# Optimization experiments

Hardware: AMD Instinct MI355X
Metric: run time of the kernel (lower is better)

## Reference

```python
import jax, jax.numpy as jnp
import numpy as np

C64 = jnp.complex64


def _ry(t):  # scalar angle -> [2,2] complex
    c = jnp.cos(t / 2).astype(C64)
    s = jnp.sin(t / 2).astype(C64)
    return jnp.stack([jnp.stack([c, -s]), jnp.stack([s, c])])


def _rz(t):  # scalar angle -> [2,2] complex (diagonal)
    p = jnp.exp(-0.5j * t.astype(C64))
    z = jnp.zeros((), C64)
    return jnp.stack([jnp.stack([p, z]), jnp.stack([z, jnp.conj(p)])])


def _rx_batch(t):  # t: [B] -> [B,2,2] complex (per-sample RX encoding gate)
    c = jnp.cos(t / 2).astype(C64)
    s = jnp.sin(t / 2).astype(C64)
    row0 = jnp.stack([c, -1j * s], axis=-1)
    row1 = jnp.stack([-1j * s, c], axis=-1)
    return jnp.stack([row0, row1], axis=-2)


def _apply_1q(state, gate, wire, n):
    # state: [B, 2^n]; wire 0 is the most significant bit (PennyLane convention)
    B = state.shape[0]
    pre, post = 2 ** wire, 2 ** (n - wire - 1)
    s = state.reshape(B, pre, 2, post)
    if gate.ndim == 2:
        s = jnp.einsum('ij,bpjq->bpiq', gate, s)
    else:  # per-sample gate [B,2,2]
        s = jnp.einsum('bij,bpjq->bpiq', gate, s)
    return s.reshape(B, -1)


def _apply_cnot(state, wire, n):
    # CNOT with control=wire, target=wire+1 (adjacent wires)
    B = state.shape[0]
    pre, post = 2 ** wire, 2 ** (n - wire - 2)
    s = state.reshape(B, pre, 2, 2, post)
    # control==1 block gets its target axis flipped
    s = jnp.concatenate([s[:, :, :1], s[:, :, 1:, ::-1]], axis=2)
    return s.reshape(B, -1)


def _circuit(x, params):
    # Batched statevector simulation of: RX(x_i) encoding, then n_layers of
    # (RY,RZ,RY) per wire + CNOT chain, then <Z_i> per wire.
    B, n = x.shape
    L = params.shape[0]
    state = jnp.zeros((B, 2 ** n), C64).at[:, 0].set(1.0)
    for i in range(n):
        state = _apply_1q(state, _rx_batch(x[:, i]), i, n)
    for l in range(L):
        for i in range(n):
            # RY(p0) first, then RZ(p1), then RY(p2): fuse into one 2x2 gate
            g = _ry(params[l, i, 2]) @ _rz(params[l, i, 1]) @ _ry(params[l, i, 0])
            state = _apply_1q(state, g, i, n)
        for i in range(n - 1):
            state = _apply_cnot(state, i, n)
    probs = jnp.abs(state) ** 2  # [B, 2^n] float32
    ez = []
    for i in range(n):
        p = probs.reshape(B, 2 ** i, 2, 2 ** (n - i - 1))
        ez.append(p[:, :, 0].sum((1, 2)) - p[:, :, 1].sum((1, 2)))
    return jnp.stack(ez, axis=1)  # [B, n]


def setup_inputs() -> dict:
    key = jax.random.key(0)
    k1, k2, k3, _ = jax.random.split(key, 4)
    B, n, L = 8192, 12, 3
    return {
        'x': jax.random.normal(k1, (B, n), jnp.float32),
        'params': jax.random.normal(k2, (L, n, 3), jnp.float32),
        'head_w': jax.random.normal(k3, (1, n), jnp.float32) / np.float32(np.sqrt(n)),
        'head_b': jnp.zeros((1,), jnp.float32),
    }


def reference(x, params, head_w, head_b):
    ez = _circuit(x, params)           # [B, n] per-wire Z expectations
    out = ez @ head_w.T + head_b       # Linear(n, 1)
    return out[:, 0]                   # squeeze(-1) -> [B]
```

## Files before the change

### kernel.cpp

```cpp
#include <hip/hip_runtime.h>
#include <math.h>

#define NQ 12
#define NTH 512
#define NL 3
#define GRID 768

typedef _Float16 h8 __attribute__((ext_vector_type(8)));
typedef _Float16 h4 __attribute__((ext_vector_type(4)));
typedef float f4 __attribute__((ext_vector_type(4)));


__device__ __forceinline__ int sfx(int v) {
    v ^= v >> 1; v ^= v >> 2; v ^= v >> 4; v ^= v >> 8;
    return v;
}
__device__ __forceinline__ int swzf(int off) {
    return off ^ (((((off >> 6) ^ (off >> 9)) & 7)) << 3);
}
__device__ __forceinline__ int swzw(int off) {
    return off ^ (((off >> 6) & 7) << 3);
}


__global__ void __launch_bounds__(NTH)
qsim_kernel(const float* __restrict__ x,
            const float* __restrict__ params,
            const float* __restrict__ head_w,
            const float* __restrict__ head_b,
            float* __restrict__ out, int Btot) {
    __shared__ __align__(16) _Float16 Sst[16384];
    __shared__ __align__(16) _Float16 Wl[9216];
    __shared__ float wlo[64], whi[64];
    __shared__ float csx[6 * 24], snx[6 * 24];
    __shared__ float wred[16];
    float* Gs = (float*)Sst;

    const int t = threadIdx.x, blk = blockIdx.x;
    const int npairs = (Btot + 1) >> 1;

    if (t < 36) {
        float p0 = params[t * 3 + 0], p1 = params[t * 3 + 1], p2 = params[t * 3 + 2];
        float c0 = cosf(0.5f * p0), s0 = sinf(0.5f * p0);
        float ch = cosf(0.5f * p1), sh = sinf(0.5f * p1);
        float c2 = cosf(0.5f * p2), s2 = sinf(0.5f * p2);
        float pr = ch, pi = -sh, qr = ch, qi = sh;
        float A = c2 * c0, Bc = s2 * s0, Cc = c2 * s0, D = s2 * c0;
        float* g = &Gs[t * 8];
        g[0] = A * pr - Bc * qr;  g[1] = A * pi - Bc * qi;
        g[2] = -Cc * pr - D * qr; g[3] = -Cc * pi - D * qi;
        g[4] = D * pr + Cc * qr;  g[5] = D * pi + Cc * qi;
        g[6] = -Bc * pr + A * qr; g[7] = -Bc * pi + A * qi;
    }
    if (t >= 64 && t < 208) {
        int idx = t - 64;
        int pr = idx / 24, w = idx - pr * 24;
        int pairIdx = blk + pr * GRID;
        if (pairIdx < npairs) {
            int smp = pairIdx * 2 + (w >= 12 ? 1 : 0);
            int wire = (w >= 12) ? (w - 12) : w;
            if (smp < Btot) {
                float xv = 0.5f * x[smp * NQ + wire];
                csx[pr * 24 + w] = cosf(xv);
                snx[pr * 24 + w] = sinf(xv);
            }
        }
    }
    if (t >= 256 && t < 320) {
        int v = t - 256; float s = 0.f;
#pragma unroll
        for (int be = 0; be < 6; ++be)
            s += ((v >> be) & 1) ? -head_w[11 - be] : head_w[11 - be];
        wlo[v] = s;
    }
    if (t >= 320 && t < 384) {
        int v = t - 320; float s = 0.f;
#pragma unroll
        for (int be = 0; be < 6; ++be)
            s += ((v >> be) & 1) ? -head_w[5 - be] : head_w[5 - be];
        whi[v] = s;
    }
    __syncthreads();

#pragma unroll
    for (int i = 0; i < 18; ++i) {
        int e = i * 512 + t;
        int s = e >> 10, idx = e & 1023;
        int n = idx >> 5, k = idx & 31;
        int rp = n >> 4, tp = n & 15, rr = k >> 4, tt = k & 15;
        int l = s / 3, g = s - 3 * l;
        float ur = 1.f, ui = 0.f;
#pragma unroll
        for (int jj = 0; jj < 4; ++jj) {
            int wire = 11 - (4 * g + jj);
            const float* gp = &Gs[(l * 12 + wire) * 8];
            int rb = (tp >> jj) & 1, cb = (tt >> jj) & 1;
            float gr = gp[(rb * 2 + cb) * 2], gi = gp[(rb * 2 + cb) * 2 + 1];
            float nr = ur * gr - ui * gi;
            float ni = ur * gi + ui * gr;
            ur = nr; ui = ni;
        }
        float val = (rp == 0) ? ((rr == 0) ? ur : -ui)
                              : ((rr == 0) ? ui : ur);
        Wl[swzw(e)] = (_Float16)val;
    }
    __syncthreads();

    const int u = t & 15, q = (t >> 4) & 3, wv = t >> 6;
    const int abase0 = swzf((wv * 16 + u) * 32 + q * 8);
    const int abase1 = swzf(((wv + 8) * 16 + u) * 32 + q * 8);
    const int wbs = swzw(u * 32 + q * 8);
    const int wv3 = wv & 3, wvh = wv >> 2;
    const int mf0 = (wv3 | (u << 2) | (wvh << 6)) * 32;
    const int mf1 = (wv3 | (u << 2) | ((wvh + 2) << 6)) * 32;
    const int s00 = swzf(mf0 + q * 4), s01 = swzf(mf0 + 16 + q * 4);
    const int s10 = swzf(mf1 + q * 4), s11 = swzf(mf1 + 16 + q * 4);
    const int p4 = (wv * 4 + q) & 15;
    const int bm = (p4 | (u << 4)) * 32 + (wv >> 2) * 4;
    const int b00 = swzf(bm), b01 = swzf(bm + 16), b10 = swzf(bm + 8), b11 = swzf(bm + 24);
    const int j0a = sfx(u * 256 + wv * 16 + q * 4);
    const int j0b = sfx(u * 256 + (wv + 8) * 16 + q * 4);
    const int cca = j0a & 3, ccb = j0b & 3;
    const int ea = cca ^ (cca >> 1), eb = ccb ^ (ccb >> 1);
    const int jba = j0a ^ cca, jbb = j0b ^ ccb;
    const int obA = ((jba >> 4) << 5) | (jba & 12);
    const int obB = ((jbb >> 4) << 5) | (jbb & 12);
    const int pA0 = swzf(obA), pA1 = swzf(obA + 16);
    const int pB0 = swzf(obB), pB1 = swzf(obB + 16);
    const float wha = whi[j0a >> 6], whb = whi[j0b >> 6];
    const int jla = j0a & 63, jlb = j0b & 63;
    const float W0a = wlo[jla] + wha, W1a = wlo[jla ^ 1] + wha;
    const float W2a = wlo[jla ^ 3] + wha, W3a = wlo[jla ^ 2] + wha;
    const float W0b = wlo[jlb] + whb, W1b = wlo[jlb ^ 1] + whb;
    const float W2b = wlo[jlb ^ 3] + whb, W3b = wlo[jlb ^ 2] + whb;
    const f4 Z = {0.f, 0.f, 0.f, 0.f};

#define STH(off_, c_) { h4 w_;                                               \
    w_.x = (_Float16)(c_).x; w_.y = (_Float16)(c_).y;                        \
    w_.z = (_Float16)(c_).z; w_.w = (_Float16)(c_).w;                        \
    *(h4*)&Sst[off_] = w_; }

#define PSTH(off_, SOFF_, e_, v_) {                                          \
    bool e1_ = ((e_) & 1), e2_ = (((e_) & 2) != 0);                          \
    float b0_ = e1_ ? (v_).y : (v_).x, b1_ = e1_ ? (v_).x : (v_).y;          \
    float b2_ = e1_ ? (v_).w : (v_).z, b3_ = e1_ ? (v_).z : (v_).w;          \
    h4 w_;                                                                   \
    w_.x = (_Float16)(e2_ ? b2_ : b0_); w_.y = (_Float16)(e2_ ? b3_ : b1_);  \
    w_.z = (_Float16)(e2_ ? b1_ : b3_); w_.w = (_Float16)(e2_ ? b0_ : b2_);  \
    *(h4*)&Sst[(off_) + (SOFF_)] = w_; }

#define KSTEP_NB(sW_) {                                                      \
    h8 bf0 = *(const h8*)&Wl[(sW_) + wbs];                                   \
    h8 bf1 = *(const h8*)&Wl[(sW_) + 512 + wbs];                             \
    h8 a0A = *(const h8*)&Sst[abase0];                                       \
    h8 a1A = *(const h8*)&Sst[abase1];                                       \
    h8 a0B = *(const h8*)&Sst[abase0 + 8192];                                \
    h8 a1B = *(const h8*)&Sst[abase1 + 8192];                                \
    cA00 = __builtin_amdgcn_mfma_f32_16x16x32_f16(a0A, bf0, Z, 0, 0, 0);     \
    cA01 = __builtin_amdgcn_mfma_f32_16x16x32_f16(a0A, bf1, Z, 0, 0, 0);     \
    cA10 = __builtin_amdgcn_mfma_f32_16x16x32_f16(a1A, bf0, Z, 0, 0, 0);     \
    cA11 = __builtin_amdgcn_mfma_f32_16x16x32_f16(a1A, bf1, Z, 0, 0, 0);     \
    cB00 = __builtin_amdgcn_mfma_f32_16x16x32_f16(a0B, bf0, Z, 0, 0, 0);     \
    cB01 = __builtin_amdgcn_mfma_f32_16x16x32_f16(a0B, bf1, Z, 0, 0, 0);     \
    cB10 = __builtin_amdgcn_mfma_f32_16x16x32_f16(a1B, bf0, Z, 0, 0, 0);     \
    cB11 = __builtin_amdgcn_mfma_f32_16x16x32_f16(a1B, bf1, Z, 0, 0, 0);     \
}

#define KSTEP(sW_) { KSTEP_NB(sW_) __syncthreads(); }

#define INITS(cs_, sn_, SOFF_) {                                             \
    int m_ = t & 255, reim_ = t >> 8;                                        \
    float magm_ = 1.f;                                                       \
    _Pragma("unroll") for (int j_ = 0; j_ < 8; ++j_)                         \
        magm_ *= ((m_ >> j_) & 1) ? (sn_)[7 - j_] : (cs_)[7 - j_];           \
    float A2_[4], B2_[4];                                                    \
    _Pragma("unroll") for (int v_ = 0; v_ < 4; ++v_) {                       \
        A2_[v_] = ((v_ & 1) ? (sn_)[11] : (cs_)[11]) *                       \
                  ((v_ & 2) ? (sn_)[10] : (cs_)[10]);                        \
        B2_[v_] = ((v_ & 1) ? (sn_)[9] : (cs_)[9]) *                         \
                  ((v_ & 2) ? (sn_)[8] : (cs_)[8]);                          \
    }                                                                        \
    int pm_ = __popc(m_);                                                    \
    h8 w0_, w1_;                                                             \
    _Pragma("unroll") for (int tau_ = 0; tau_ < 16; ++tau_) {                \
        float mag_ = magm_ * A2_[tau_ & 3] * B2_[tau_ >> 2];                 \
        int p_ = (pm_ + __popc(tau_)) & 3;                                   \
        bool nz_ = ((p_ & 1) == reim_);                                      \
        bool ng_ = ((((p_ >> 1) & 1) ^ reim_) != 0);                         \
        float v_ = nz_ ? (ng_ ? -mag_ : mag_) : 0.f;                         \
        if (tau_ < 8) w0_[tau_] = (_Float16)v_; else w1_[tau_ - 8] = (_Float16)v_; \
    }                                                                        \
    int off_ = m_ * 32 + reim_ * 16;                                         \
    *(h8*)&Sst[swzf(off_) + (SOFF_)] = w0_;                                  \
    *(h8*)&Sst[swzf(off_ + 8) + (SOFF_)] = w1_; }

#pragma unroll 1
    for (int pr = 0; ; ++pr) {
        const int pairIdx = blk + pr * GRID;
        if (pairIdx >= npairs) break;
        const float* cs0 = &csx[pr * 24];
        const float* sn0 = &snx[pr * 24];
        INITS(cs0, sn0, 0)
        INITS((cs0 + 12), (sn0 + 12), 8192)
        __syncthreads();

        float racc0 = 0.f, racc1 = 0.f;
#pragma unroll
        for (int l = 0; l < NL; ++l) {
            f4 cA00, cA01, cA10, cA11, cB00, cB01, cB10, cB11;
            KSTEP((l * 3 + 0) * 1024)
            STH(s00, cA00) STH(s01, cA01) STH(s10, cA10) STH(s11, cA11)
            STH(s00 + 8192, cB00) STH(s01 + 8192, cB01)
            STH(s10 + 8192, cB10) STH(s11 + 8192, cB11)
            __syncthreads();
            KSTEP((l * 3 + 1) * 1024)
            STH(b00, cA00) STH(b01, cA01) STH(b10, cA10) STH(b11, cA11)
            STH(b00 + 8192, cB00) STH(b01 + 8192, cB01)
            STH(b10 + 8192, cB10) STH(b11 + 8192, cB11)
            __syncthreads();
            if (l < NL - 1) {
                KSTEP((l * 3 + 2) * 1024)
                PSTH(pA0, 0, ea, cA00) PSTH(pA1, 0, ea, cA01)
                PSTH(pB0, 0, eb, cA10) PSTH(pB1, 0, eb, cA11)
                PSTH(pA0, 8192, ea, cB00) PSTH(pA1, 8192, ea, cB01)
                PSTH(pB0, 8192, eb, cB10) PSTH(pB1, 8192, eb, cB11)
                __syncthreads();
            } else {
                KSTEP_NB((l * 3 + 2) * 1024)
                racc0 = fmaf(fmaf(cA00.x, cA00.x, cA01.x * cA01.x), W0a, racc0);
                racc0 = fmaf(fmaf(cA00.y, cA00.y, cA01.y * cA01.y), W1a, racc0);
                racc0 = fmaf(fmaf(cA00.z, cA00.z, cA01.z * cA01.z), W2a, racc0);
                racc0 = fmaf(fmaf(cA00.w, cA00.w, cA01.w * cA01.w), W3a, racc0);
                racc0 = fmaf(fmaf(cA10.x, cA10.x, cA11.x * cA11.x), W0b, racc0);
                racc0 = fmaf(fmaf(cA10.y, cA10.y, cA11.y * cA11.y), W1b, racc0);
                racc0 = fmaf(fmaf(cA10.z, cA10.z, cA11.z * cA11.z), W2b, racc0);
                racc0 = fmaf(fmaf(cA10.w, cA10.w, cA11.w * cA11.w), W3b, racc0);
                racc1 = fmaf(fmaf(cB00.x, cB00.x, cB01.x * cB01.x), W0a, racc1);
                racc1 = fmaf(fmaf(cB00.y, cB00.y, cB01.y * cB01.y), W1a, racc1);
                racc1 = fmaf(fmaf(cB00.z, cB00.z, cB01.z * cB01.z), W2a, racc1);
                racc1 = fmaf(fmaf(cB00.w, cB00.w, cB01.w * cB01.w), W3a, racc1);
                racc1 = fmaf(fmaf(cB10.x, cB10.x, cB11.x * cB11.x), W0b, racc1);
                racc1 = fmaf(fmaf(cB10.y, cB10.y, cB11.y * cB11.y), W1b, racc1);
                racc1 = fmaf(fmaf(cB10.z, cB10.z, cB11.z * cB11.z), W2b, racc1);
                racc1 = fmaf(fmaf(cB10.w, cB10.w, cB11.w * cB11.w), W3b, racc1);
            }
        }
#pragma unroll
        for (int o = 32; o >= 1; o >>= 1) {
            racc0 += __shfl_xor(racc0, o, 64);
            racc1 += __shfl_xor(racc1, o, 64);
        }
        if ((t & 63) == 0) { wred[wv] = racc0; wred[8 + wv] = racc1; }
        __syncthreads();
        if (t < 2) {
            int smp = pairIdx * 2 + t;
            if (smp < Btot) {
                float r = head_b[0];
#pragma unroll
                for (int i2 = 0; i2 < 8; ++i2) r += wred[t * 8 + i2];
                out[smp] = r;
            }
        }
    }
}

extern "C" void kernel_launch(void* const* d_in, const int* in_sizes, int n_in,
                              void* d_out, int out_size, void* d_ws, size_t ws_size,
                              hipStream_t stream) {
    const float* x = (const float*)d_in[0];
    const float* params = (const float*)d_in[1];
    const float* head_w = (const float*)d_in[2];
    const float* head_b = (const float*)d_in[3];
    float* out = (float*)d_out;
    int B = in_sizes[0] / NQ;

    hipLaunchKernelGGL(qsim_kernel, dim3(GRID), dim3(NTH), 0, stream,
                       x, params, head_w, head_b, out, B);
}
```

Measured before the change: 127.2 us.

## Halve block size and chain two gate stages in registers via permlane swaps

Blocks drop from 512 to 256 threads with a minimum-occupancy hint of 3, so each wave now handles four M-blocks per MFMA stage. The second and third gate-group matmuls in each layer are chained in registers using v_permlane32/16 swaps to transpose the MFMA output into the next A-operand. This removes one shared-memory store, reload and barrier round trip per layer. It adds register pressure and relies on gfx950-specific permlane swap instructions and a new swizzle and index mapping, which raises the risk of layout errors.

```diff
diff --git a/kernel.cpp b/kernel.cpp
--- a/kernel.cpp
+++ b/kernel.cpp
@@ -2,28 +2,46 @@
 #include <math.h>
 
 #define NQ 12
-#define NTH 512
+#define NTH 256
 #define NL 3
 #define GRID 768
 
 typedef _Float16 h8 __attribute__((ext_vector_type(8)));
 typedef _Float16 h4 __attribute__((ext_vector_type(4)));
+typedef _Float16 hf2 __attribute__((ext_vector_type(2)));
 typedef float f4 __attribute__((ext_vector_type(4)));
 
-
-__device__ __forceinline__ int sfx(int v) {
-    v ^= v >> 1; v ^= v >> 2; v ^= v >> 4; v ^= v >> 8;
-    return v;
-}
+#define MFMA __builtin_amdgcn_mfma_f32_16x16x32_f16
+
+
 __device__ __forceinline__ int swzf(int off) {
     return off ^ (((((off >> 6) ^ (off >> 9)) & 7)) << 3);
 }
+__device__ __forceinline__ int swz1(int off) {
+    return off ^ ((((off >> 5) ^ (off >> 9)) & 7) << 3);
+}
 __device__ __forceinline__ int swzw(int off) {
     return off ^ (((off >> 6) & 7) << 3);
 }
 
-
-__global__ void __launch_bounds__(NTH)
+__device__ __forceinline__ unsigned pk2(float lo, float hi) {
+    hf2 t_; t_.x = (_Float16)lo; t_.y = (_Float16)hi;
+    unsigned r_; __builtin_memcpy(&r_, &t_, 4); return r_;
+}
+
+__device__ __forceinline__ h8 xition(f4 re, f4 im) {
+    unsigned a0 = pk2(re.x, re.y), a1 = pk2(re.z, re.w);
+    unsigned b0 = pk2(im.x, im.y), b1 = pk2(im.z, im.w);
+    asm("v_permlane32_swap_b32 %0, %1" : "+v"(a0), "+v"(b0));
+    asm("v_permlane16_swap_b32 %0, %1" : "+v"(a0), "+v"(b0));
+    asm("v_permlane32_swap_b32 %0, %1" : "+v"(a1), "+v"(b1));
+    asm("v_permlane16_swap_b32 %0, %1" : "+v"(a1), "+v"(b1));
+    union { unsigned u[4]; h8 v; } r_;
+    r_.u[0] = a0; r_.u[1] = a1; r_.u[2] = b0; r_.u[3] = b1;
+    return r_.v;
+}
+
+__global__ void __launch_bounds__(NTH, 3)
 qsim_kernel(const float* __restrict__ x,
             const float* __restrict__ params,
             const float* __restrict__ head_w,
@@ -33,7 +51,7 @@
     __shared__ __align__(16) _Float16 Wl[9216];
     __shared__ float wlo[64], whi[64];
     __shared__ float csx[6 * 24], snx[6 * 24];
-    __shared__ float wred[16];
+    __shared__ float wred[8];
     float* Gs = (float*)Sst;
 
     const int t = threadIdx.x, blk = blockIdx.x;
@@ -44,16 +62,16 @@
         float c0 = cosf(0.5f * p0), s0 = sinf(0.5f * p0);
         float ch = cosf(0.5f * p1), sh = sinf(0.5f * p1);
         float c2 = cosf(0.5f * p2), s2 = sinf(0.5f * p2);
-        float pr = ch, pi = -sh, qr = ch, qi = sh;
+        float pr_ = ch, pi = -sh, qr = ch, qi = sh;
         float A = c2 * c0, Bc = s2 * s0, Cc = c2 * s0, D = s2 * c0;
         float* g = &Gs[t * 8];
-        g[0] = A * pr - Bc * qr;  g[1] = A * pi - Bc * qi;
-        g[2] = -Cc * pr - D * qr; g[3] = -Cc * pi - D * qi;
-        g[4] = D * pr + Cc * qr;  g[5] = D * pi + Cc * qi;
-        g[6] = -Bc * pr + A * qr; g[7] = -Bc * pi + A * qi;
-    }
-    if (t >= 64 && t < 208) {
-        int idx = t - 64;
+        g[0] = A * pr_ - Bc * qr;  g[1] = A * pi - Bc * qi;
+        g[2] = -Cc * pr_ - D * qr; g[3] = -Cc * pi - D * qi;
+        g[4] = D * pr_ + Cc * qr;  g[5] = D * pi + Cc * qi;
+        g[6] = -Bc * pr_ + A * qr; g[7] = -Bc * pi + A * qi;
+    }
+    if (t >= 36 && t < 180) {
+        int idx = t - 36;
         int pr = idx / 24, w = idx - pr * 24;
         int pairIdx = blk + pr * GRID;
         if (pairIdx < npairs) {
@@ -66,25 +84,20 @@
             }
         }
     }
-    if (t >= 256 && t < 320) {
-        int v = t - 256; float s = 0.f;
-#pragma unroll
-        for (int be = 0; be < 6; ++be)
-            s += ((v >> be) & 1) ? -head_w[11 - be] : head_w[11 - be];
-        wlo[v] = s;
-    }
-    if (t >= 320 && t < 384) {
-        int v = t - 320; float s = 0.f;
-#pragma unroll
-        for (int be = 0; be < 6; ++be)
-            s += ((v >> be) & 1) ? -head_w[5 - be] : head_w[5 - be];
-        whi[v] = s;
+    if (t >= 192) {
+        int v = t - 192; float s = 0.f, s2 = 0.f;
+#pragma unroll
+        for (int be = 0; be < 6; ++be) {
+            s  += ((v >> be) & 1) ? -head_w[11 - be] : head_w[11 - be];
+            s2 += ((v >> be) & 1) ? -head_w[5 - be]  : head_w[5 - be];
+        }
+        wlo[v] = s; whi[v] = s2;
     }
     __syncthreads();
 
 #pragma unroll
-    for (int i = 0; i < 18; ++i) {
-        int e = i * 512 + t;
+    for (int i = 0; i < 36; ++i) {
+        int e = i * 256 + t;
         int s = e >> 10, idx = e & 1023;
         int n = idx >> 5, k = idx & 31;
         int rp = n >> 4, tp = n & 15, rr = k >> 4, tt = k & 15;
@@ -106,70 +119,79 @@
     }
     __syncthreads();
 
-    const int u = t & 15, q = (t >> 4) & 3, wv = t >> 6;
-    const int abase0 = swzf((wv * 16 + u) * 32 + q * 8);
-    const int abase1 = swzf(((wv + 8) * 16 + u) * 32 + q * 8);
+    const int wv = t >> 6, u = t & 15, q = (t >> 4) & 3;
     const int wbs = swzw(u * 32 + q * 8);
-    const int wv3 = wv & 3, wvh = wv >> 2;
-    const int mf0 = (wv3 | (u << 2) | (wvh << 6)) * 32;
-    const int mf1 = (wv3 | (u << 2) | ((wvh + 2) << 6)) * 32;
-    const int s00 = swzf(mf0 + q * 4), s01 = swzf(mf0 + 16 + q * 4);
-    const int s10 = swzf(mf1 + q * 4), s11 = swzf(mf1 + 16 + q * 4);
-    const int p4 = (wv * 4 + q) & 15;
-    const int bm = (p4 | (u << 4)) * 32 + (wv >> 2) * 4;
-    const int b00 = swzf(bm), b01 = swzf(bm + 16), b10 = swzf(bm + 8), b11 = swzf(bm + 24);
-    const int j0a = sfx(u * 256 + wv * 16 + q * 4);
-    const int j0b = sfx(u * 256 + (wv + 8) * 16 + q * 4);
-    const int cca = j0a & 3, ccb = j0b & 3;
-    const int ea = cca ^ (cca >> 1), eb = ccb ^ (ccb >> 1);
-    const int jba = j0a ^ cca, jbb = j0b ^ ccb;
-    const int obA = ((jba >> 4) << 5) | (jba & 12);
-    const int obB = ((jbb >> 4) << 5) | (jbb & 12);
-    const int pA0 = swzf(obA), pA1 = swzf(obA + 16);
-    const int pB0 = swzf(obB), pB1 = swzf(obB + 16);
-    const float wha = whi[j0a >> 6], whb = whi[j0b >> 6];
-    const int jla = j0a & 63, jlb = j0b & 63;
-    const float W0a = wlo[jla] + wha, W1a = wlo[jla ^ 1] + wha;
-    const float W2a = wlo[jla ^ 3] + wha, W3a = wlo[jla ^ 2] + wha;
-    const float W0b = wlo[jlb] + whb, W1b = wlo[jlb ^ 1] + whb;
-    const float W2b = wlo[jlb ^ 3] + whb, W3b = wlo[jlb ^ 2] + whb;
+    int g0b[4], g1b[4];
+#pragma unroll
+    for (int mb = 0; mb < 4; ++mb) {
+        int m_ = wv * 64 + (u >> 2) * 16 + mb * 4 + (u & 3);
+        g0b[mb] = swzf(m_ * 32 + q * 8);
+        int l_ = t & 63;
+        int m1 = ((l_ >> 2) & 3) * 64 + (l_ & 3) * 16 + wv * 4 + mb;
+        g1b[mb] = swz1(m1 * 32 + q * 8);
+    }
+    const int sb = (t * 32) ^ (((t ^ (t >> 4)) & 7) << 3);
+
+    const int s4 = (u ^ (u >> 1) ^ (u >> 2) ^ (u >> 3)) & 15;
+    const int P4 = s4 & 1, q0 = q & 1, q1 = q >> 1;
+    const int j7 = q1 ^ P4, j6 = q0 ^ q1 ^ P4;
+    const int wv0 = wv & 1, wv1 = wv >> 1;
+    int Eo[4], PwR[4];
+#pragma unroll
+    for (int r = 0; r < 4; ++r) {
+        int r0 = r & 1, r1 = r >> 1;
+        int j5 = r1 ^ j6, j4 = (r0 ^ r1) ^ j6;
+        int j3 = wv1 ^ j4, j2 = wv0 ^ wv1 ^ j4;
+        int m0 = s4 * 16 + j7 * 8 + j6 * 4 + j5 * 2 + j4;
+        Eo[r]  = swzf(m0 * 32 + j3 * 8 + j2 * 4);
+        PwR[r] = (wv0 ^ wv1 ^ j4);
+    }
+    const int Pw0 = wv0 ^ wv1 ^ j6;
+    const int wloB = j6 * 48 + (wv1 ^ j6) * 8 + (wv0 ^ wv1 ^ j6) * 4 + Pw0 * 3;
+    const float whiv = whi[s4 * 4 + j7 * 2 + j6];
     const f4 Z = {0.f, 0.f, 0.f, 0.f};
 
-#define STH(off_, c_) { h4 w_;                                               \
-    w_.x = (_Float16)(c_).x; w_.y = (_Float16)(c_).y;                        \
-    w_.z = (_Float16)(c_).z; w_.w = (_Float16)(c_).w;                        \
-    *(h4*)&Sst[off_] = w_; }
-
-#define PSTH(off_, SOFF_, e_, v_) {                                          \
-    bool e1_ = ((e_) & 1), e2_ = (((e_) & 2) != 0);                          \
-    float b0_ = e1_ ? (v_).y : (v_).x, b1_ = e1_ ? (v_).x : (v_).y;          \
-    float b2_ = e1_ ? (v_).w : (v_).z, b3_ = e1_ ? (v_).z : (v_).w;          \
-    h4 w_;                                                                   \
-    w_.x = (_Float16)(e2_ ? b2_ : b0_); w_.y = (_Float16)(e2_ ? b3_ : b1_);  \
-    w_.z = (_Float16)(e2_ ? b1_ : b3_); w_.w = (_Float16)(e2_ ? b0_ : b2_);  \
-    *(h4*)&Sst[(off_) + (SOFF_)] = w_; }
-
-#define KSTEP_NB(sW_) {                                                      \
-    h8 bf0 = *(const h8*)&Wl[(sW_) + wbs];                                   \
-    h8 bf1 = *(const h8*)&Wl[(sW_) + 512 + wbs];                             \
-    h8 a0A = *(const h8*)&Sst[abase0];                                       \
-    h8 a1A = *(const h8*)&Sst[abase1];                                       \
-    h8 a0B = *(const h8*)&Sst[abase0 + 8192];                                \
-    h8 a1B = *(const h8*)&Sst[abase1 + 8192];                                \
-    cA00 = __builtin_amdgcn_mfma_f32_16x16x32_f16(a0A, bf0, Z, 0, 0, 0);     \
-    cA01 = __builtin_amdgcn_mfma_f32_16x16x32_f16(a0A, bf1, Z, 0, 0, 0);     \
-    cA10 = __builtin_amdgcn_mfma_f32_16x16x32_f16(a1A, bf0, Z, 0, 0, 0);     \
-    cA11 = __builtin_amdgcn_mfma_f32_16x16x32_f16(a1A, bf1, Z, 0, 0, 0);     \
-    cB00 = __builtin_amdgcn_mfma_f32_16x16x32_f16(a0B, bf0, Z, 0, 0, 0);     \
-    cB01 = __builtin_amdgcn_mfma_f32_16x16x32_f16(a0B, bf1, Z, 0, 0, 0);     \
-    cB10 = __builtin_amdgcn_mfma_f32_16x16x32_f16(a1B, bf0, Z, 0, 0, 0);     \
-    cB11 = __builtin_amdgcn_mfma_f32_16x16x32_f16(a1B, bf1, Z, 0, 0, 0);     \
-}
-
-#define KSTEP(sW_) { KSTEP_NB(sW_) __syncthreads(); }
+#define ST16(off_, va_, vb_) { h8 w_;                                        \
+    w_[0] = (_Float16)(va_).x; w_[1] = (_Float16)(va_).y;                    \
+    w_[2] = (_Float16)(va_).z; w_[3] = (_Float16)(va_).w;                    \
+    w_[4] = (_Float16)(vb_).x; w_[5] = (_Float16)(vb_).y;                    \
+    w_[6] = (_Float16)(vb_).z; w_[7] = (_Float16)(vb_).w;                    \
+    *(h8*)&Sst[off_] = w_; }
+
+#define PST1(CMP_, r_) {                                                     \
+    bool pw_ = PwR[r_] != 0;                                                 \
+    { float v0=eRA[0].CMP_, v1=eRA[1].CMP_, v2=eRA[2].CMP_, v3=eRA[3].CMP_;  \
+      h4 w_; w_.x=(_Float16)(pw_?v2:v0); w_.y=(_Float16)(pw_?v3:v1);         \
+             w_.z=(_Float16)(pw_?v1:v3); w_.w=(_Float16)(pw_?v0:v2);         \
+      *(h4*)&Sst[Eo[r_]] = w_; }                                             \
+    { float v0=eIA[0].CMP_, v1=eIA[1].CMP_, v2=eIA[2].CMP_, v3=eIA[3].CMP_;  \
+      h4 w_; w_.x=(_Float16)(pw_?v2:v0); w_.y=(_Float16)(pw_?v3:v1);         \
+             w_.z=(_Float16)(pw_?v1:v3); w_.w=(_Float16)(pw_?v0:v2);         \
+      *(h4*)&Sst[Eo[r_] ^ 16] = w_; }                                        \
+    { float v0=eRB[0].CMP_, v1=eRB[1].CMP_, v2=eRB[2].CMP_, v3=eRB[3].CMP_;  \
+      h4 w_; w_.x=(_Float16)(pw_?v2:v0); w_.y=(_Float16)(pw_?v3:v1);         \
+             w_.z=(_Float16)(pw_?v1:v3); w_.w=(_Float16)(pw_?v0:v2);         \
+      *(h4*)&Sst[Eo[r_] + 8192] = w_; }                                      \
+    { float v0=eIB[0].CMP_, v1=eIB[1].CMP_, v2=eIB[2].CMP_, v3=eIB[3].CMP_;  \
+      h4 w_; w_.x=(_Float16)(pw_?v2:v0); w_.y=(_Float16)(pw_?v3:v1);         \
+             w_.z=(_Float16)(pw_?v1:v3); w_.w=(_Float16)(pw_?v0:v2);         \
+      *(h4*)&Sst[(Eo[r_] ^ 16) + 8192] = w_; } }
+
+#define RD1(CMP_, dr_) {                                                     \
+    int b_ = wloB ^ (dr_);                                                   \
+    float w0_ = whiv + wlo[b_],     w1_ = whiv + wlo[b_ ^ 1];                \
+    float w2_ = whiv + wlo[b_ ^ 3], w3_ = whiv + wlo[b_ ^ 2];                \
+    racc0 = fmaf(fmaf(eRA[0].CMP_, eRA[0].CMP_, eIA[0].CMP_*eIA[0].CMP_), w0_, racc0); \
+    racc0 = fmaf(fmaf(eRA[1].CMP_, eRA[1].CMP_, eIA[1].CMP_*eIA[1].CMP_), w1_, racc0); \
+    racc0 = fmaf(fmaf(eRA[2].CMP_, eRA[2].CMP_, eIA[2].CMP_*eIA[2].CMP_), w2_, racc0); \
+    racc0 = fmaf(fmaf(eRA[3].CMP_, eRA[3].CMP_, eIA[3].CMP_*eIA[3].CMP_), w3_, racc0); \
+    racc1 = fmaf(fmaf(eRB[0].CMP_, eRB[0].CMP_, eIB[0].CMP_*eIB[0].CMP_), w0_, racc1); \
+    racc1 = fmaf(fmaf(eRB[1].CMP_, eRB[1].CMP_, eIB[1].CMP_*eIB[1].CMP_), w1_, racc1); \
+    racc1 = fmaf(fmaf(eRB[2].CMP_, eRB[2].CMP_, eIB[2].CMP_*eIB[2].CMP_), w2_, racc1); \
+    racc1 = fmaf(fmaf(eRB[3].CMP_, eRB[3].CMP_, eIB[3].CMP_*eIB[3].CMP_), w3_, racc1); }
 
 #define INITS(cs_, sn_, SOFF_) {                                             \
-    int m_ = t & 255, reim_ = t >> 8;                                        \
+    int m_ = t;                                                              \
     float magm_ = 1.f;                                                       \
     _Pragma("unroll") for (int j_ = 0; j_ < 8; ++j_)                         \
         magm_ *= ((m_ >> j_) & 1) ? (sn_)[7 - j_] : (cs_)[7 - j_];           \
@@ -181,18 +203,20 @@
                   ((v_ & 2) ? (sn_)[8] : (cs_)[8]);                          \
     }                                                                        \
     int pm_ = __popc(m_);                                                    \
-    h8 w0_, w1_;                                                             \
-    _Pragma("unroll") for (int tau_ = 0; tau_ < 16; ++tau_) {                \
-        float mag_ = magm_ * A2_[tau_ & 3] * B2_[tau_ >> 2];                 \
-        int p_ = (pm_ + __popc(tau_)) & 3;                                   \
-        bool nz_ = ((p_ & 1) == reim_);                                      \
-        bool ng_ = ((((p_ >> 1) & 1) ^ reim_) != 0);                         \
-        float v_ = nz_ ? (ng_ ? -mag_ : mag_) : 0.f;                         \
-        if (tau_ < 8) w0_[tau_] = (_Float16)v_; else w1_[tau_ - 8] = (_Float16)v_; \
-    }                                                                        \
-    int off_ = m_ * 32 + reim_ * 16;                                         \
-    *(h8*)&Sst[swzf(off_) + (SOFF_)] = w0_;                                  \
-    *(h8*)&Sst[swzf(off_ + 8) + (SOFF_)] = w1_; }
+    _Pragma("unroll") for (int reim_ = 0; reim_ < 2; ++reim_) {              \
+        h8 w0_, w1_;                                                         \
+        _Pragma("unroll") for (int tau_ = 0; tau_ < 16; ++tau_) {            \
+            float mag_ = magm_ * A2_[tau_ & 3] * B2_[tau_ >> 2];             \
+            int p_ = (pm_ + __popc(tau_)) & 3;                               \
+            bool nz_ = ((p_ & 1) == reim_);                                  \
+            bool ng_ = ((((p_ >> 1) & 1) ^ reim_) != 0);                     \
+            float v_ = nz_ ? (ng_ ? -mag_ : mag_) : 0.f;                     \
+            if (tau_ < 8) w0_[tau_] = (_Float16)v_; else w1_[tau_ - 8] = (_Float16)v_; \
+        }                                                                    \
+        int off_ = m_ * 32 + reim_ * 16;                                     \
+        *(h8*)&Sst[swzf(off_) + (SOFF_)] = w0_;                              \
+        *(h8*)&Sst[swzf(off_ + 8) + (SOFF_)] = w1_;                          \
+    } }
 
 #pragma unroll 1
     for (int pr = 0; ; ++pr) {
@@ -207,42 +231,84 @@
         float racc0 = 0.f, racc1 = 0.f;
 #pragma unroll
         for (int l = 0; l < NL; ++l) {
-            f4 cA00, cA01, cA10, cA11, cB00, cB01, cB10, cB11;
-            KSTEP((l * 3 + 0) * 1024)
-            STH(s00, cA00) STH(s01, cA01) STH(s10, cA10) STH(s11, cA11)
-            STH(s00 + 8192, cB00) STH(s01 + 8192, cB01)
-            STH(s10 + 8192, cB10) STH(s11 + 8192, cB11)
-            __syncthreads();
-            KSTEP((l * 3 + 1) * 1024)
-            STH(b00, cA00) STH(b01, cA01) STH(b10, cA10) STH(b11, cA11)
-            STH(b00 + 8192, cB00) STH(b01 + 8192, cB01)
-            STH(b10 + 8192, cB10) STH(b11 + 8192, cB11)
-            __syncthreads();
-            if (l < NL - 1) {
-                KSTEP((l * 3 + 2) * 1024)
-                PSTH(pA0, 0, ea, cA00) PSTH(pA1, 0, ea, cA01)
-                PSTH(pB0, 0, eb, cA10) PSTH(pB1, 0, eb, cA11)
-                PSTH(pA0, 8192, ea, cB00) PSTH(pA1, 8192, ea, cB01)
-                PSTH(pB0, 8192, eb, cB10) PSTH(pB1, 8192, eb, cB11)
+            {
+                const int sW = (l * 3 + 0) * 1024;
+                h8 bf0 = *(const h8*)&Wl[sW + wbs];
+                h8 bf1 = *(const h8*)&Wl[sW + 512 + wbs];
+                h8 aA[4], aB[4];
+#pragma unroll
+                for (int mb = 0; mb < 4; ++mb) {
+                    aA[mb] = *(const h8*)&Sst[g0b[mb]];
+                    aB[mb] = *(const h8*)&Sst[g0b[mb] + 8192];
+                }
                 __syncthreads();
-            } else {
-                KSTEP_NB((l * 3 + 2) * 1024)
-                racc0 = fmaf(fmaf(cA00.x, cA00.x, cA01.x * cA01.x), W0a, racc0);
-                racc0 = fmaf(fmaf(cA00.y, cA00.y, cA01.y * cA01.y), W1a, racc0);
-                racc0 = fmaf(fmaf(cA00.z, cA00.z, cA01.z * cA01.z), W2a, racc0);
-                racc0 = fmaf(fmaf(cA00.w, cA00.w, cA01.w * cA01.w), W3a, racc0);
-                racc0 = fmaf(fmaf(cA10.x, cA10.x, cA11.x * cA11.x), W0b, racc0);
-                racc0 = fmaf(fmaf(cA10.y, cA10.y, cA11.y * cA11.y), W1b, racc0);
-                racc0 = fmaf(fmaf(cA10.z, cA10.z, cA11.z * cA11.z), W2b, racc0);
-                racc0 = fmaf(fmaf(cA10.w, cA10.w, cA11.w * cA11.w), W3b, racc0);
-                racc1 = fmaf(fmaf(cB00.x, cB00.x, cB01.x * cB01.x), W0a, racc1);
-                racc1 = fmaf(fmaf(cB00.y, cB00.y, cB01.y * cB01.y), W1a, racc1);
-                racc1 = fmaf(fmaf(cB00.z, cB00.z, cB01.z * cB01.z), W2a, racc1);
-                racc1 = fmaf(fmaf(cB00.w, cB00.w, cB01.w * cB01.w), W3a, racc1);
-                racc1 = fmaf(fmaf(cB10.x, cB10.x, cB11.x * cB11.x), W0b, racc1);
-                racc1 = fmaf(fmaf(cB10.y, cB10.y, cB11.y * cB11.y), W1b, racc1);
-                racc1 = fmaf(fmaf(cB10.z, cB10.z, cB11.z * cB11.z), W2b, racc1);
-                racc1 = fmaf(fmaf(cB10.w, cB10.w, cB11.w * cB11.w), W3b, racc1);
+                f4 cR[4], cI[4];
+#pragma unroll
+                for (int mb = 0; mb < 4; ++mb) {
+                    cR[mb] = MFMA(aA[mb], bf0, Z, 0, 0, 0);
+                    cI[mb] = MFMA(aA[mb], bf1, Z, 0, 0, 0);
+                }
+                ST16(sb,        cR[0], cR[1]) ST16(sb ^ 8,  cR[2], cR[3])
+                ST16(sb ^ 16,   cI[0], cI[1]) ST16(sb ^ 24, cI[2], cI[3])
+#pragma unroll
+                for (int mb = 0; mb < 4; ++mb) {
+                    cR[mb] = MFMA(aB[mb], bf0, Z, 0, 0, 0);
+                    cI[mb] = MFMA(aB[mb], bf1, Z, 0, 0, 0);
+                }
+                ST16(sb + 8192,        cR[0], cR[1]) ST16((sb ^ 8) + 8192,  cR[2], cR[3])
+                ST16((sb ^ 16) + 8192, cI[0], cI[1]) ST16((sb ^ 24) + 8192, cI[2], cI[3])
+                __syncthreads();
+            }
+            {
+                const int sW1 = (l * 3 + 1) * 1024, sW2 = (l * 3 + 2) * 1024;
+                h8 bg0 = *(const h8*)&Wl[sW1 + wbs];
+                h8 bg1 = *(const h8*)&Wl[sW1 + 512 + wbs];
+                h8 bh0 = *(const h8*)&Wl[sW2 + wbs];
+                h8 bh1 = *(const h8*)&Wl[sW2 + 512 + wbs];
+                h8 gA[4], gB[4];
+#pragma unroll
+                for (int mb = 0; mb < 4; ++mb) {
+                    gA[mb] = *(const h8*)&Sst[g1b[mb]];
+                    gB[mb] = *(const h8*)&Sst[g1b[mb] + 8192];
+                }
+                if (l < NL - 1) __syncthreads();
+                f4 eRA[4], eIA[4], eRB[4], eIB[4];
+                {
+                    f4 dR[4], dI[4]; h8 t2[4];
+#pragma unroll
+                    for (int mb = 0; mb < 4; ++mb) {
+                        dR[mb] = MFMA(gA[mb], bg0, Z, 0, 0, 0);
+                        dI[mb] = MFMA(gA[mb], bg1, Z, 0, 0, 0);
+                    }
+#pragma unroll
+                    for (int mb = 0; mb < 4; ++mb) t2[mb] = xition(dR[mb], dI[mb]);
+#pragma unroll
+                    for (int mb = 0; mb < 4; ++mb) {
+                        eRA[mb] = MFMA(t2[mb], bh0, Z, 0, 0, 0);
+                        eIA[mb] = MFMA(t2[mb], bh1, Z, 0, 0, 0);
+                    }
+                }
+                {
+                    f4 dR[4], dI[4]; h8 t2[4];
+#pragma unroll
+                    for (int mb = 0; mb < 4; ++mb) {
+                        dR[mb] = MFMA(gB[mb], bg0, Z, 0, 0, 0);
+                        dI[mb] = MFMA(gB[mb], bg1, Z, 0, 0, 0);
+                    }
+#pragma unroll
+                    for (int mb = 0; mb < 4; ++mb) t2[mb] = xition(dR[mb], dI[mb]);
+#pragma unroll
+                    for (int mb = 0; mb < 4; ++mb) {
+                        eRB[mb] = MFMA(t2[mb], bh0, Z, 0, 0, 0);
+                        eIB[mb] = MFMA(t2[mb], bh1, Z, 0, 0, 0);
+                    }
+                }
+                if (l < NL - 1) {
+                    PST1(x, 0) PST1(y, 1) PST1(z, 2) PST1(w, 3)
+                    __syncthreads();
+                } else {
+                    RD1(x, 0) RD1(y, 31) RD1(z, 63) RD1(w, 32)
+                }
             }
         }
 #pragma unroll
@@ -250,14 +316,14 @@
             racc0 += __shfl_xor(racc0, o, 64);
             racc1 += __shfl_xor(racc1, o, 64);
         }
-        if ((t & 63) == 0) { wred[wv] = racc0; wred[8 + wv] = racc1; }
+        if ((t & 63) == 0) { wred[wv] = racc0; wred[4 + wv] = racc1; }
         __syncthreads();
         if (t < 2) {
             int smp = pairIdx * 2 + t;
             if (smp < Btot) {
                 float r = head_b[0];
 #pragma unroll
-                for (int i2 = 0; i2 < 8; ++i2) r += wred[t * 8 + i2];
+                for (int i2 = 0; i2 < 4; ++i2) r += wred[t * 4 + i2];
                 out[smp] = r;
             }
         }
```

Measured after the change: 121.2 us. -4.7%, faster.
